# Kernel optimization log

Measured on AMD Instinct MI355X. Metric: run time of the kernel, lower is better.

The kernel has to match this reference:

```python
import jax, jax.numpy as jnp
from jax import lax
import numpy as np

B, W, V, E, H = 512, 40, 12000, 512, 512


def setup_inputs() -> dict:
    key = jax.random.key(0)
    ks = jax.random.split(key, 9)
    s = 0.05
    ques_vec = jax.random.randint(ks[0], (B, W), 0, V + 1)          # token ids, 0 = pad
    ques_len = jax.random.randint(ks[1], (B,), 1, W + 1)             # valid lengths in [1, W]
    lookup_W = jax.random.normal(ks[2], (E, V), jnp.float32) * s     # nn.Linear(vocab, emb).weight
    wih0 = jax.random.normal(ks[3], (2, 4 * H, E), jnp.float32) * s  # [dir, 4H, in]
    whh0 = jax.random.normal(ks[4], (2, 4 * H, H), jnp.float32) * s
    b0 = jax.random.normal(ks[5], (2, 2, 4 * H), jnp.float32) * s    # [dir, {b_ih,b_hh}, 4H]
    wih1 = jax.random.normal(ks[6], (2, 4 * H, 2 * H), jnp.float32) * s
    whh1 = jax.random.normal(ks[7], (2, 4 * H, H), jnp.float32) * s
    b1 = jax.random.normal(ks[8], (2, 2, 4 * H), jnp.float32) * s
    return {"ques_vec": ques_vec, "ques_len": ques_len, "lookup_W": lookup_W,
            "wih0": wih0, "whh0": whh0, "b0": b0,
            "wih1": wih1, "whh1": whh1, "b1": b1}


def _lstm_dir(x, wih, whh, b, reverse):
    # x: [B, T, D]; PyTorch gate order i, f, g, o
    Hc = whh.shape[1]
    xg = jnp.einsum('btd,gd->btg', x, wih) + b[0] + b[1]  # [B, T, 4H]
    xs = jnp.swapaxes(xg, 0, 1)                            # [T, B, 4H]
    if reverse:
        xs = xs[::-1]

    def step(carry, g_t):
        h, c = carry
        g = g_t + h @ whh.T
        i, f, gg, o = jnp.split(g, 4, axis=-1)
        c = jax.nn.sigmoid(f) * c + jax.nn.sigmoid(i) * jnp.tanh(gg)
        h = jax.nn.sigmoid(o) * jnp.tanh(c)
        return (h, c), h

    h0 = jnp.zeros((x.shape[0], Hc), x.dtype)
    _, hs = lax.scan(step, (h0, h0), xs)
    if reverse:
        hs = hs[::-1]
    return jnp.swapaxes(hs, 0, 1)  # [B, T, H]


def _bilstm(x, wih, whh, b):
    fwd = _lstm_dir(x, wih[0], whh[0], b[0], False)
    bwd = _lstm_dir(x, wih[1], whh[1], b[1], True)
    return jnp.concatenate([fwd, bwd], axis=-1)  # [B, T, 2H]


def reference(ques_vec, ques_len, lookup_W, wih0, whh0, b0, wih1, whh1, b1):
    # one-hot over vocab+1 with column 0 dropped == gather with id 0 -> zero vector
    table = jnp.concatenate([jnp.zeros((1, E), lookup_W.dtype), lookup_W.T], axis=0)  # [V+1, E]
    emb = jnp.tanh(table[ques_vec])          # [B, W, E] (dropout=0 -> identity)
    h = _bilstm(emb, wih0, whh0, b0)         # layer 0
    h = _bilstm(h, wih1, whh1, b1)           # layer 1 -> [B, W, 2H]
    # scatter-mask bmm == select hidden state at timestep ques_len-1
    idx = (ques_len - 1)[:, None, None]
    return jnp.take_along_axis(h, idx, axis=1).reshape(ques_vec.shape[0], -1)  # [B, 2H]
```

## Files before the change

### kernel.cpp

```cpp
#include <hip/hip_runtime.h>
#include <hip/hip_bf16.h>
#include <stdint.h>

#define NB 512
#define NW 40
#define NE 512
#define NH 512
#define NV 12000
#define G4 2048

typedef unsigned short u16;
typedef unsigned int u32;
typedef unsigned long long u64;
typedef __attribute__((ext_vector_type(8))) short short8;
typedef __attribute__((ext_vector_type(4))) float f32x4;

__device__ __forceinline__ unsigned short f2bf(float f) {
  unsigned int u = __float_as_uint(f);
  u += 0x7FFF + ((u >> 16) & 1);
  return (unsigned short)(u >> 16);
}
__device__ __forceinline__ float bf2f(unsigned short b) {
  return __uint_as_float(((unsigned int)b) << 16);
}
__device__ __forceinline__ float loadIn(const void* p, long i, int bf) {
  return bf ? bf2f(((const u16*)p)[i]) : ((const float*)p)[i];
}

__global__ void detect_kernel(const u16* p, int* flag) {
  __shared__ int cnt;
  int i = threadIdx.x;
  if (i == 0) cnt = 0;
  __syncthreads();
  unsigned short u = p[2 * (i * 1001)];
  int e = (u >> 7) & 0xFF;
  if (e >= 100 && e <= 126) atomicAdd(&cnt, 1);
  __syncthreads();
  if (i == 0) *flag = (cnt >= 32) ? 1 : 0;
}

__global__ void table_kernel(const void* lookup, const int* flag, u16* tableT) {
  __shared__ float tile[64][65];
  int bf = *flag;
  int v0 = blockIdx.x * 64, e0 = blockIdx.y * 64;
  int tx = threadIdx.x, ty = threadIdx.y;
#pragma unroll
  for (int r = 0; r < 16; ++r) {
    int e = r * 4 + ty, v = tx;
    if (v0 + v < NV)
      tile[e][v] = tanhf(loadIn(lookup, (long)(e0 + e) * NV + v0 + v, bf));
  }
  __syncthreads();
#pragma unroll
  for (int r = 0; r < 16; ++r) {
    int v = r * 4 + ty, e = tx;
    if (v0 + v < NV)
      tableT[(long)(v0 + v) * NE + e0 + e] = f2bf(tile[e][v]);
  }
}

__global__ void embed_kernel(const int* __restrict__ qv,
                             const u16* __restrict__ tableT,
                             u16* __restrict__ emb) {
  int tid = blockIdx.x * 256 + threadIdx.x;
  int token = tid >> 6;
  int chunk = tid & 63;
  int tt = token / NB, b = token % NB;
  int q = qv[b * NW + tt];
  uint4 val = make_uint4(0u, 0u, 0u, 0u);
  if (q > 0) val = *(const uint4*)(tableT + (long)(q - 1) * NE + chunk * 8);
  *(uint4*)(emb + (long)token * NE + chunk * 8) = val;
}

__global__ void pack_kernel(const void* wih0, const void* whh0, const void* b0,
                            const void* wih1, const void* whh1, const void* b1,
                            const int* flag, u16* Wc0, u16* Wc1, float* bsum) {
  const long N0 = 2L * G4 * 1024, N1 = 2L * G4 * 1536;
  long idx = (long)blockIdx.x * 256 + threadIdx.x;
  int bf = *flag;
  if (idx < N0) {
    int d = (int)(idx / (G4 * 1024));
    int rem = (int)(idx % (long)(G4 * 1024));
    int g = rem / 1024, k = rem % 1024;
    float v = (k < 512) ? loadIn(wih0, ((long)d * G4 + g) * 512 + k, bf)
                        : loadIn(whh0, ((long)d * G4 + g) * 512 + (k - 512), bf);
    Wc0[idx] = f2bf(v);
  } else if (idx < N0 + N1) {
    long i2 = idx - N0;
    int d = (int)(i2 / (G4 * 1536));
    int rem = (int)(i2 % (long)(G4 * 1536));
    int g = rem / 1536, k = rem % 1536;
    float v = (k < 1024) ? loadIn(wih1, ((long)d * G4 + g) * 1024 + k, bf)
                         : loadIn(whh1, ((long)d * G4 + g) * 512 + (k - 1024), bf);
    Wc1[i2] = f2bf(v);
  } else if (idx < N0 + N1 + 2L * 2 * G4) {
    long i3 = idx - N0 - N1;
    int layer = (int)(i3 / (2 * G4));
    int d = (int)((i3 / G4) & 1);
    int g = (int)(i3 % G4);
    const void* bb = layer ? b1 : b0;
    float v = loadIn(bb, (long)d * 2 * G4 + g, bf) +
              loadIn(bb, (long)d * 2 * G4 + G4 + g, bf);
    bsum[i3] = v;
  }
}

__global__ void zero_bar(unsigned int* bar) {
  bar[blockIdx.x * 256 + threadIdx.x] = 0u;
}

__global__ __launch_bounds__(256, 2) void xg_gemm(
    const u16* __restrict__ X, int Kx, int Kfull, const u16* __restrict__ Wc,
    const float* __restrict__ bsumL, u16* __restrict__ xg) {
  __shared__ __align__(16) char lds[32768];
  const int tid = threadIdx.x;
  const int lane = tid & 63, wv = tid >> 6;
  const int wm = wv & 1, wn = wv >> 1;
  const int col = lane & 15, quad = lane >> 4;
  const int s = blockIdx.x >> 5, w = blockIdx.x & 31;
  const int bx = (s % 40) * 4 + (w & 3);
  const int by = (s / 40) * 8 + (w >> 2);
  const int tb0 = bx * 128;
  const int d = by >> 4, colb = by & 15, j0 = colb * 32;

  f32x4 zero = {0.f, 0.f, 0.f, 0.f};
  f32x4 acc[4][4];
#pragma unroll
  for (int i = 0; i < 4; ++i)
#pragma unroll
    for (int j = 0; j < 4; ++j) acc[i][j] = zero;

  const int iters = Kx >> 6;
  for (int it = 0; it < iters; ++it) {
    int k0 = it << 6;
#pragma unroll
    for (int p = 0; p < 8; ++p) {
      int c = p * 256 + tid;
      const u16* gsrc;
      if (c < 1024) {
        int r = c >> 3, sl = c & 7;
        int kk = k0 + ((sl * 8) ^ ((r & 7) << 3));
        gsrc = X + (long)(tb0 + r) * Kx + kk;
      } else {
        int cb = c - 1024;
        int r = cb >> 3, sl = cb & 7;
        int kk = k0 + ((sl * 8) ^ ((r & 7) << 3));
        int grow = (r >> 5) * 512 + j0 + (r & 31);
        gsrc = Wc + ((long)d * G4 + grow) * Kfull + kk;
      }
      __builtin_amdgcn_global_load_lds(
          (const __attribute__((address_space(1))) void*)(const void*)gsrc,
          (__attribute__((address_space(3))) void*)(lds + p * 4096 + wv * 1024),
          16, 0, 0);
    }
    __syncthreads();
    const u16* As = (const u16*)lds;
    const u16* Bs = (const u16*)(lds + 16384);
#pragma unroll
    for (int ks = 0; ks < 2; ++ks) {
      short8 afr[4], bfr[4];
#pragma unroll
      for (int mf = 0; mf < 4; ++mf) {
        int rm = wm * 64 + mf * 16 + col;
        int sl = (ks * 32 + quad * 8) ^ ((rm & 7) << 3);
        afr[mf] = *(const short8*)(As + rm * 64 + sl);
      }
#pragma unroll
      for (int nf = 0; nf < 4; ++nf) {
        int br = wn * 64 + nf * 16 + col;
        int sl = (ks * 32 + quad * 8) ^ ((br & 7) << 3);
        bfr[nf] = *(const short8*)(Bs + br * 64 + sl);
      }
#pragma unroll
      for (int mf = 0; mf < 4; ++mf)
#pragma unroll
        for (int nf = 0; nf < 4; ++nf)
          acc[mf][nf] = __builtin_amdgcn_mfma_f32_16x16x32_bf16(
              afr[mf], bfr[nf], acc[mf][nf], 0, 0, 0);
    }
    __syncthreads();
  }

  float bias[4];
#pragma unroll
  for (int nf = 0; nf < 4; ++nf) {
    int n = wn * 64 + nf * 16 + col;
    bias[nf] = bsumL[d * G4 + (n >> 5) * 512 + j0 + (n & 31)];
  }
#pragma unroll
  for (int mf = 0; mf < 4; ++mf)
#pragma unroll
    for (int nf = 0; nf < 4; ++nf) {
      int n = wn * 64 + nf * 16 + col;
      int g = n >> 5, jn = n & 31;
#pragma unroll
      for (int r = 0; r < 4; ++r) {
        int m = wm * 64 + mf * 16 + quad * 4 + r;
        int tb = tb0 + m, t = tb >> 9, b = tb & 511;
        long oi = ((((long)t * 2 + d) * 16 + colb) * 512 + b) * 128 + jn * 4 + g;
        xg[oi] = f2bf(acc[mf][nf][r] + bias[nf]);
      }
    }
}

__global__ __launch_bounds__(256, 1) void lstm_pers(
    const u16* __restrict__ xg, const u16* __restrict__ Wc, int Kfull, int Kx,
    u16* __restrict__ hbuf, u16* __restrict__ h0cat, void* __restrict__ outp,
    const int* __restrict__ qlen, const int* __restrict__ flag,
    unsigned int* bar, int layer) {
  __shared__ __align__(16) char lds[163840];
  const int tid = threadIdx.x;
  const int lane = tid & 63, wv = tid >> 6;
  const int wm = wv & 1, wn = wv >> 1;
  const int col = lane & 15, quad = lane >> 4;
  const int l = blockIdx.x;
  const int colid = l & 31, mi = l >> 5;
  const int colb = colid & 15, j0 = colb * 32, d = colid >> 4;
  const int m0 = mi * 64;
  const int gid = l >> 4;

#pragma unroll
  for (int p = 0; p < 32; ++p) {
    int c = p * 256 + tid;
    int row = c >> 6, rem = c & 63;
    int kc = rem >> 3, sl = rem & 7;
    int grow = (row >> 5) * 512 + j0 + (row & 31);
    int gk = Kx + kc * 64 + ((sl * 8) ^ ((row & 7) << 3));
    const u16* gsrc = Wc + ((long)d * G4 + grow) * Kfull + gk;
    __builtin_amdgcn_global_load_lds(
        (const __attribute__((address_space(1))) void*)(const void*)gsrc,
        (__attribute__((address_space(3))) void*)(lds + p * 4096 + wv * 1024),
        16, 0, 0);
  }
  const u16* Bs = (const u16*)lds;
  char* hstg = lds + 131072;
  u16* hLDS = (u16*)hstg;

  float creg[2][4];
#pragma unroll
  for (int i = 0; i < 2; ++i)
#pragma unroll
    for (int r = 0; r < 4; ++r) creg[i][r] = 0.f;
  const int isbf = *flag;
  f32x4 zero = {0.f, 0.f, 0.f, 0.f};

  __syncthreads();

#pragma unroll 1
  for (int t = 0; t < NW; ++t) {
    const int tq = d ? (NW - 1 - t) : t;

    ushort4 xgv[2][4];
    const u16* xgt = xg + ((((long)tq * 2 + d) * 16 + colb) * 512 + m0) * 128;
#pragma unroll
    for (int mf = 0; mf < 2; ++mf)
#pragma unroll
      for (int r = 0; r < 4; ++r) {
        int m = wm * 32 + mf * 16 + quad * 4 + r;
        xgv[mf][r] = *(const ushort4*)(xgt + m * 128 + (wn * 16 + col) * 4);
      }

    f32x4 acc[2][4];
#pragma unroll
    for (int i = 0; i < 2; ++i)
#pragma unroll
      for (int j = 0; j < 4; ++j) acc[i][j] = zero;

    if (t > 0) {
      const u16* hp =
          hbuf + ((t - 1) & 1) * (2L * NB * NH) + ((long)d * NB + m0) * NH;
      auto stage = [&](int it, int pb) {
        char* dst = hstg + pb * 16384;
#pragma unroll
        for (int p = 0; p < 4; ++p) {
          int c = p * 256 + tid;
          int row = c >> 4, slot = c & 15;
          int half = slot >> 3, ck = slot & 7;
          int kk = it * 128 + half * 64 + ((ck * 8) ^ ((row & 7) << 3));
          const u16* gsrc = hp + (long)row * NH + kk;
          __builtin_amdgcn_global_load_lds(
              (const __attribute__((address_space(1))) void*)(const void*)gsrc,
              (__attribute__((address_space(3))) void*)(dst + p * 4096 +
                                                        wv * 1024),
              16, 0, 16 );
        }
      };
      stage(0, 0);
      __syncthreads();
#pragma unroll 1
      for (int it = 0; it < 4; ++it) {
        if (it + 1 < 4) stage(it + 1, (it + 1) & 1);
        const u16* As = (const u16*)(hstg + (it & 1) * 16384);
#pragma unroll
        for (int ks = 0; ks < 4; ++ks) {
          short8 afr[2], bfr[4];
          const int ksub = ks * 32 + quad * 8;
#pragma unroll
          for (int mf = 0; mf < 2; ++mf) {
            int rm = wm * 32 + mf * 16 + col;
            int sl = (ksub & 63) ^ ((rm & 7) << 3);
            afr[mf] = *(const short8*)(As + rm * 128 + (ksub & 64) + sl);
          }
          const int kc = it * 128 + ksub;
#pragma unroll
          for (int g = 0; g < 4; ++g) {
            int br = g * 32 + wn * 16 + col;
            int sl = (kc & 63) ^ ((br & 7) << 3);
            bfr[g] = *(const short8*)(Bs + br * 512 + (kc & ~63) + sl);
          }
#pragma unroll
          for (int mf = 0; mf < 2; ++mf)
#pragma unroll
            for (int g = 0; g < 4; ++g)
              acc[mf][g] = __builtin_amdgcn_mfma_f32_16x16x32_bf16(
                  afr[mf], bfr[g], acc[mf][g], 0, 0, 0);
        }
        if (it + 1 < 4) __syncthreads();
      }
    }

#pragma unroll
    for (int mf = 0; mf < 2; ++mf)
#pragma unroll
      for (int r = 0; r < 4; ++r) {
        int m = wm * 32 + mf * 16 + quad * 4 + r;
        const u16* xv = (const u16*)&xgv[mf][r];
        float gi = acc[mf][0][r] + bf2f(xv[0]);
        float gf = acc[mf][1][r] + bf2f(xv[1]);
        float gg = acc[mf][2][r] + bf2f(xv[2]);
        float go = acc[mf][3][r] + bf2f(xv[3]);
        float si = 1.f / (1.f + __expf(-gi));
        float sf = 1.f / (1.f + __expf(-gf));
        float so = 1.f / (1.f + __expf(-go));
        float cn = sf * creg[mf][r] + si * tanhf(gg);
        float h = so * tanhf(cn);
        creg[mf][r] = cn;
        hLDS[m * 32 + wn * 16 + col] = f2bf(h);
        if (layer == 1 && !isbf) {
          int bg = m0 + m;
          if (qlen[bg] - 1 == tq)
            ((float*)outp)[(long)bg * (2 * NH) + d * NH + j0 + wn * 16 + col] =
                h;
        }
      }
    __syncthreads();

    u16* hnxt = hbuf + (t & 1) * (2L * NB * NH);
#pragma unroll
    for (int p = 0; p < 4; ++p) {
      int c = p * 256 + tid;
      int m = c >> 4, pr = c & 15;
      u32 hw = ((const u32*)hLDS)[m * 16 + pr];
      int bg = m0 + m, jg = j0 + pr * 2;
      __hip_atomic_store((u32*)(hnxt + ((long)d * NB + bg) * NH + jg), hw,
                         __ATOMIC_RELAXED, __HIP_MEMORY_SCOPE_AGENT);
      if (layer == 0) {
        *(u32*)(h0cat + ((long)tq * NB + bg) * (2 * NH) + d * NH + jg) = hw;
      } else if (isbf && qlen[bg] - 1 == tq) {
        *(u32*)((u16*)outp + (long)bg * (2 * NH) + d * NH + jg) = hw;
      }
    }

    if (t < NW - 1) {
      __syncthreads();
      if (tid == 0) {
        u32* cnt = &bar[gid * 64];
        u32* flg = &bar[1024 + gid * 64];
        unsigned old = __hip_atomic_fetch_add(cnt, 1u, __ATOMIC_RELAXED,
                                              __HIP_MEMORY_SCOPE_AGENT);
        if (old == 16u * (t + 1) - 1u)
          __hip_atomic_store(flg, (unsigned)(t + 1), __ATOMIC_RELAXED,
                             __HIP_MEMORY_SCOPE_AGENT);
        else
          while (__hip_atomic_load(flg, __ATOMIC_RELAXED,
                                   __HIP_MEMORY_SCOPE_AGENT) <
                 (unsigned)(t + 1))
            __builtin_amdgcn_s_sleep(1);
      }
      __syncthreads();
    }
  }
}

extern "C" void kernel_launch(void* const* d_in, const int* in_sizes, int n_in,
                              void* d_out, int out_size, void* d_ws,
                              size_t ws_size, hipStream_t stream) {
  const int* qv = (const int*)d_in[0];
  const int* ql = (const int*)d_in[1];
  const void* lookup = d_in[2];
  const void* wih0 = d_in[3];
  const void* whh0 = d_in[4];
  const void* b0 = d_in[5];
  const void* wih1 = d_in[6];
  const void* whh1 = d_in[7];
  const void* b1 = d_in[8];

  char* ws = (char*)d_ws;
  size_t off = 0;
  int* flag = (int*)ws;                 off += 256;
  unsigned int* bar = (unsigned int*)(ws + off); off += 8192;
  float* bsum = (float*)(ws + off);     off += 2L * 2 * G4 * 4;
  u16* Wc0 = (u16*)(ws + off);          off += 2L * G4 * 1024 * 2;
  u16* Wc1 = (u16*)(ws + off);          off += 2L * G4 * 1536 * 2;
  u16* hbuf = (u16*)(ws + off);         off += 2L * 2 * NB * NH * 2;
  u16* h0cat = (u16*)(ws + off);        off += (size_t)NW * NB * 2 * NH * 2;
  u16* emb = (u16*)(ws + off);          off += (size_t)NW * NB * NE * 2;
  u16* xg = (u16*)(ws + off);           off += (size_t)NW * 2 * 16 * 512 * 128 * 2;
  u16* tableT = h0cat;

  detect_kernel<<<1, 64, 0, stream>>>((const u16*)lookup, flag);
  table_kernel<<<dim3(188, 8), dim3(64, 4), 0, stream>>>(lookup, flag, tableT);
  {
    long total = 2L * G4 * 1024 + 2L * G4 * 1536 + 2L * 2 * G4;
    int blocks = (int)((total + 255) / 256);
    pack_kernel<<<blocks, 256, 0, stream>>>(wih0, whh0, b0, wih1, whh1, b1,
                                            flag, Wc0, Wc1, bsum);
  }
  embed_kernel<<<NW * NB / 4, 256, 0, stream>>>(qv, tableT, emb);

  xg_gemm<<<5120, 256, 0, stream>>>(emb, 512, 1024, Wc0, bsum, xg);
  zero_bar<<<8, 256, 0, stream>>>(bar);
  lstm_pers<<<256, 256, 0, stream>>>(xg, Wc0, 1024, 512, hbuf, h0cat, d_out,
                                     ql, flag, bar, 0);
  xg_gemm<<<5120, 256, 0, stream>>>(h0cat, 1024, 1536, Wc1, bsum + 2 * G4, xg);
  zero_bar<<<8, 256, 0, stream>>>(bar);
  lstm_pers<<<256, 256, 0, stream>>>(xg, Wc1, 1536, 1024, hbuf, h0cat, d_out,
                                     ql, flag, bar, 1);
}
```

Before: 1.000 ms.

## Interleave both LSTM directions per block with per-block flag barrier and register-loaded h

Each block now owns 16 hidden columns for both directions and alternates forward and backward steps. The second direction's work can then overlap the first direction's wait on its barrier. The centralized atomic-counter barrier is replaced by per-block flags that one wave polls with a ballot. Hidden state is loaded straight from global memory into registers instead of being staged through double-buffered LDS. Sigmoid and tanh now use fast reciprocal/exp approximations, trading some accuracy for fewer instructions. The barrier flag layout and the block-to-column mapping change, which relies on the launch and workspace setup matching.

```diff
diff --git a/kernel.cpp b/kernel.cpp
--- a/kernel.cpp
+++ b/kernel.cpp
@@ -25,6 +25,14 @@
 }
 __device__ __forceinline__ float loadIn(const void* p, long i, int bf) {
   return bf ? bf2f(((const u16*)p)[i]) : ((const float*)p)[i];
+}
+__device__ __forceinline__ float fast_tanh(float x) {
+  float ax = __builtin_fabsf(x);
+  float t = 1.f - 2.f * __builtin_amdgcn_rcpf(__expf(ax + ax) + 1.f);
+  return __builtin_copysignf(t, x);
+}
+__device__ __forceinline__ float sigm(float x) {
+  return __builtin_amdgcn_rcpf(1.f + __expf(-x));
 }
 
 __global__ void detect_kernel(const u16* p, int* flag) {
@@ -208,33 +216,32 @@
     u16* __restrict__ hbuf, u16* __restrict__ h0cat, void* __restrict__ outp,
     const int* __restrict__ qlen, const int* __restrict__ flag,
     unsigned int* bar, int layer) {
-  __shared__ __align__(16) char lds[163840];
+  __shared__ __align__(16) char lds[133120];
   const int tid = threadIdx.x;
   const int lane = tid & 63, wv = tid >> 6;
-  const int wm = wv & 1, wn = wv >> 1;
   const int col = lane & 15, quad = lane >> 4;
   const int l = blockIdx.x;
-  const int colid = l & 31, mi = l >> 5;
-  const int colb = colid & 15, j0 = colb * 32, d = colid >> 4;
+  const int colb = l & 31;
+  const int mi = l >> 5;
+  const int j0 = colb * 16;
   const int m0 = mi * 64;
-  const int gid = l >> 4;
 
 #pragma unroll
   for (int p = 0; p < 32; ++p) {
     int c = p * 256 + tid;
     int row = c >> 6, rem = c & 63;
     int kc = rem >> 3, sl = rem & 7;
-    int grow = (row >> 5) * 512 + j0 + (row & 31);
+    int dr = row >> 6;
+    int grow = ((row >> 4) & 3) * 512 + j0 + (row & 15);
     int gk = Kx + kc * 64 + ((sl * 8) ^ ((row & 7) << 3));
-    const u16* gsrc = Wc + ((long)d * G4 + grow) * Kfull + gk;
+    const u16* gsrc = Wc + ((long)dr * G4 + grow) * Kfull + gk;
     __builtin_amdgcn_global_load_lds(
         (const __attribute__((address_space(1))) void*)(const void*)gsrc,
         (__attribute__((address_space(3))) void*)(lds + p * 4096 + wv * 1024),
         16, 0, 0);
   }
   const u16* Bs = (const u16*)lds;
-  char* hstg = lds + 131072;
-  u16* hLDS = (u16*)hstg;
+  u16* hLDS = (u16*)(lds + 131072);
 
   float creg[2][4];
 #pragma unroll
@@ -248,136 +255,112 @@
 
 #pragma unroll 1
   for (int t = 0; t < NW; ++t) {
-    const int tq = d ? (NW - 1 - t) : t;
-
-    ushort4 xgv[2][4];
-    const u16* xgt = xg + ((((long)tq * 2 + d) * 16 + colb) * 512 + m0) * 128;
-#pragma unroll
-    for (int mf = 0; mf < 2; ++mf)
+#pragma unroll
+    for (int d = 0; d < 2; ++d) {
+      const int tq = d ? (NW - 1 - t) : t;
+      const int gid = mi * 2 + d;
+
+      ushort4 xgv[4];
+      const u16* xgt =
+          xg + ((((long)tq * 2 + d) * 16 + (colb >> 1)) * 512 + m0) * 128;
 #pragma unroll
       for (int r = 0; r < 4; ++r) {
-        int m = wm * 32 + mf * 16 + quad * 4 + r;
-        xgv[mf][r] = *(const ushort4*)(xgt + m * 128 + (wn * 16 + col) * 4);
-      }
-
-    f32x4 acc[2][4];
-#pragma unroll
-    for (int i = 0; i < 2; ++i)
-#pragma unroll
-      for (int j = 0; j < 4; ++j) acc[i][j] = zero;
-
-    if (t > 0) {
-      const u16* hp =
-          hbuf + ((t - 1) & 1) * (2L * NB * NH) + ((long)d * NB + m0) * NH;
-      auto stage = [&](int it, int pb) {
-        char* dst = hstg + pb * 16384;
-#pragma unroll
-        for (int p = 0; p < 4; ++p) {
-          int c = p * 256 + tid;
-          int row = c >> 4, slot = c & 15;
-          int half = slot >> 3, ck = slot & 7;
-          int kk = it * 128 + half * 64 + ((ck * 8) ^ ((row & 7) << 3));
-          const u16* gsrc = hp + (long)row * NH + kk;
-          __builtin_amdgcn_global_load_lds(
-              (const __attribute__((address_space(1))) void*)(const void*)gsrc,
-              (__attribute__((address_space(3))) void*)(dst + p * 4096 +
-                                                        wv * 1024),
-              16, 0, 16 );
+        int m = wv * 16 + quad * 4 + r;
+        xgv[r] = *(const ushort4*)(xgt + m * 128 + ((colb & 1) * 16 + col) * 4);
+      }
+
+      f32x4 acc[4];
+#pragma unroll
+      for (int g = 0; g < 4; ++g) acc[g] = zero;
+
+      if (t > 0) {
+        if (wv == 0) {
+          u32* sp = bar + gid * 32 + (lane & 31);
+          while (__ballot((int)(__hip_atomic_load(sp, __ATOMIC_RELAXED,
+                                                  __HIP_MEMORY_SCOPE_AGENT) <
+                                (u32)t)))
+            __builtin_amdgcn_s_sleep(1);
         }
-      };
-      stage(0, 0);
-      __syncthreads();
-#pragma unroll 1
-      for (int it = 0; it < 4; ++it) {
-        if (it + 1 < 4) stage(it + 1, (it + 1) & 1);
-        const u16* As = (const u16*)(hstg + (it & 1) * 16384);
-#pragma unroll
-        for (int ks = 0; ks < 4; ++ks) {
-          short8 afr[2], bfr[4];
-          const int ksub = ks * 32 + quad * 8;
-#pragma unroll
-          for (int mf = 0; mf < 2; ++mf) {
-            int rm = wm * 32 + mf * 16 + col;
-            int sl = (ksub & 63) ^ ((rm & 7) << 3);
-            afr[mf] = *(const short8*)(As + rm * 128 + (ksub & 64) + sl);
+        __syncthreads();
+
+        const u16* hp = hbuf + ((t - 1) & 1) * (2L * NB * NH) +
+                        ((long)d * NB + m0 + wv * 16 + col) * NH;
+        short8 afr[16];
+#pragma unroll
+        for (int it = 0; it < 4; ++it)
+#pragma unroll
+          for (int ks = 0; ks < 4; ++ks) {
+            const u64* p = (const u64*)(hp + it * 128 + ks * 32 + quad * 8);
+            union {
+              short8 v;
+              u64 q[2];
+            } u;
+            u.q[0] = __hip_atomic_load((u64*)p, __ATOMIC_RELAXED,
+                                       __HIP_MEMORY_SCOPE_AGENT);
+            u.q[1] = __hip_atomic_load((u64*)p + 1, __ATOMIC_RELAXED,
+                                       __HIP_MEMORY_SCOPE_AGENT);
+            afr[it * 4 + ks] = u.v;
           }
-          const int kc = it * 128 + ksub;
-#pragma unroll
-          for (int g = 0; g < 4; ++g) {
-            int br = g * 32 + wn * 16 + col;
-            int sl = (kc & 63) ^ ((br & 7) << 3);
-            bfr[g] = *(const short8*)(Bs + br * 512 + (kc & ~63) + sl);
+#pragma unroll
+        for (int it = 0; it < 4; ++it)
+#pragma unroll
+          for (int ks = 0; ks < 4; ++ks) {
+            const int kc = it * 128 + ks * 32 + quad * 8;
+#pragma unroll
+            for (int g = 0; g < 4; ++g) {
+              int br = d * 64 + g * 16 + col;
+              int slb = (kc & 63) ^ ((br & 7) << 3);
+              short8 bfr = *(const short8*)(Bs + br * 512 + (kc & ~63) + slb);
+              acc[g] = __builtin_amdgcn_mfma_f32_16x16x32_bf16(
+                  afr[it * 4 + ks], bfr, acc[g], 0, 0, 0);
+            }
           }
-#pragma unroll
-          for (int mf = 0; mf < 2; ++mf)
-#pragma unroll
-            for (int g = 0; g < 4; ++g)
-              acc[mf][g] = __builtin_amdgcn_mfma_f32_16x16x32_bf16(
-                  afr[mf], bfr[g], acc[mf][g], 0, 0, 0);
-        }
-        if (it + 1 < 4) __syncthreads();
-      }
-    }
-
-#pragma unroll
-    for (int mf = 0; mf < 2; ++mf)
+      }
+
 #pragma unroll
       for (int r = 0; r < 4; ++r) {
-        int m = wm * 32 + mf * 16 + quad * 4 + r;
-        const u16* xv = (const u16*)&xgv[mf][r];
-        float gi = acc[mf][0][r] + bf2f(xv[0]);
-        float gf = acc[mf][1][r] + bf2f(xv[1]);
-        float gg = acc[mf][2][r] + bf2f(xv[2]);
-        float go = acc[mf][3][r] + bf2f(xv[3]);
-        float si = 1.f / (1.f + __expf(-gi));
-        float sf = 1.f / (1.f + __expf(-gf));
-        float so = 1.f / (1.f + __expf(-go));
-        float cn = sf * creg[mf][r] + si * tanhf(gg);
-        float h = so * tanhf(cn);
-        creg[mf][r] = cn;
-        hLDS[m * 32 + wn * 16 + col] = f2bf(h);
+        int m = wv * 16 + quad * 4 + r;
+        float gi = acc[0][r] + bf2f(xgv[r].x);
+        float gf = acc[1][r] + bf2f(xgv[r].y);
+        float gg = acc[2][r] + bf2f(xgv[r].z);
+        float go = acc[3][r] + bf2f(xgv[r].w);
+        float si = sigm(gi);
+        float sf = sigm(gf);
+        float so = sigm(go);
+        float cn = sf * creg[d][r] + si * fast_tanh(gg);
+        float h = so * fast_tanh(cn);
+        creg[d][r] = cn;
+        hLDS[m * 16 + col] = f2bf(h);
         if (layer == 1 && !isbf) {
           int bg = m0 + m;
           if (qlen[bg] - 1 == tq)
-            ((float*)outp)[(long)bg * (2 * NH) + d * NH + j0 + wn * 16 + col] =
-                h;
+            ((float*)outp)[(long)bg * (2 * NH) + d * NH + j0 + col] = h;
         }
       }
-    __syncthreads();
-
-    u16* hnxt = hbuf + (t & 1) * (2L * NB * NH);
-#pragma unroll
-    for (int p = 0; p < 4; ++p) {
-      int c = p * 256 + tid;
-      int m = c >> 4, pr = c & 15;
-      u32 hw = ((const u32*)hLDS)[m * 16 + pr];
-      int bg = m0 + m, jg = j0 + pr * 2;
-      __hip_atomic_store((u32*)(hnxt + ((long)d * NB + bg) * NH + jg), hw,
-                         __ATOMIC_RELAXED, __HIP_MEMORY_SCOPE_AGENT);
-      if (layer == 0) {
-        *(u32*)(h0cat + ((long)tq * NB + bg) * (2 * NH) + d * NH + jg) = hw;
-      } else if (isbf && qlen[bg] - 1 == tq) {
-        *(u32*)((u16*)outp + (long)bg * (2 * NH) + d * NH + jg) = hw;
-      }
-    }
-
-    if (t < NW - 1) {
       __syncthreads();
-      if (tid == 0) {
-        u32* cnt = &bar[gid * 64];
-        u32* flg = &bar[1024 + gid * 64];
-        unsigned old = __hip_atomic_fetch_add(cnt, 1u, __ATOMIC_RELAXED,
-                                              __HIP_MEMORY_SCOPE_AGENT);
-        if (old == 16u * (t + 1) - 1u)
-          __hip_atomic_store(flg, (unsigned)(t + 1), __ATOMIC_RELAXED,
-                             __HIP_MEMORY_SCOPE_AGENT);
-        else
-          while (__hip_atomic_load(flg, __ATOMIC_RELAXED,
-                                   __HIP_MEMORY_SCOPE_AGENT) <
-                 (unsigned)(t + 1))
-            __builtin_amdgcn_s_sleep(1);
-      }
-      __syncthreads();
+
+      u16* hnxt = hbuf + (t & 1) * (2L * NB * NH);
+#pragma unroll
+      for (int p = 0; p < 2; ++p) {
+        int c = p * 256 + tid;
+        int m = c >> 3, pr = c & 7;
+        u32 hw = ((const u32*)hLDS)[m * 8 + pr];
+        int bg = m0 + m, jg = j0 + pr * 2;
+        __hip_atomic_store((u32*)(hnxt + ((long)d * NB + bg) * NH + jg), hw,
+                           __ATOMIC_RELAXED, __HIP_MEMORY_SCOPE_AGENT);
+        if (layer == 0) {
+          *(u32*)(h0cat + ((long)tq * NB + bg) * (2 * NH) + d * NH + jg) = hw;
+        } else if (isbf && qlen[bg] - 1 == tq) {
+          *(u32*)((u16*)outp + (long)bg * (2 * NH) + d * NH + jg) = hw;
+        }
+      }
+
+      if (t < NW - 1) {
+        __syncthreads();
+        if (tid == 0)
+          __hip_atomic_store(bar + gid * 32 + colb, (u32)(t + 1),
+                             __ATOMIC_RELAXED, __HIP_MEMORY_SCOPE_AGENT);
+      }
     }
   }
 }
```

Result: slower. 1.265 ms (+26.5%).

## Fuse input projection GEMM into persistent LSTM kernel with MFMA-fragment layouts

Applied to the files above, without the earlier changes.

Removes the separate xg_gemm kernels and computes each timestep's input-gate projection inside the persistent LSTM kernel, overlapped after the h write and before the grid barrier. Embeddings and layer-0 outputs are written directly in MFMA fragment order, and part of W_ih (or a pre-packed layer-1 slice) is kept in LDS. This trades the xg round trip through HBM for extra per-step MFMA work on the recurrent critical path. It also retiles the blocks to 16 hidden columns by 128 rows with 32 blocks per barrier group, and swaps in rcp-based fast sigmoid and tanh.

```diff
diff --git a/kernel.cpp b/kernel.cpp
--- a/kernel.cpp
+++ b/kernel.cpp
@@ -25,6 +25,14 @@
 }
 __device__ __forceinline__ float loadIn(const void* p, long i, int bf) {
   return bf ? bf2f(((const u16*)p)[i]) : ((const float*)p)[i];
+}
+__device__ __forceinline__ float fast_tanh(float x) {
+  float ax = __builtin_fabsf(x);
+  float t = 1.f - 2.f * __builtin_amdgcn_rcpf(__expf(ax + ax) + 1.f);
+  return __builtin_copysignf(t, x);
+}
+__device__ __forceinline__ float sigm(float x) {
+  return __builtin_amdgcn_rcpf(1.f + __expf(-x));
 }
 
 __global__ void detect_kernel(const u16* p, int* flag) {
@@ -61,21 +69,28 @@
 
 __global__ void embed_kernel(const int* __restrict__ qv,
                              const u16* __restrict__ tableT,
-                             u16* __restrict__ emb) {
-  int tid = blockIdx.x * 256 + threadIdx.x;
-  int token = tid >> 6;
-  int chunk = tid & 63;
-  int tt = token / NB, b = token % NB;
-  int q = qv[b * NW + tt];
+                             u16* __restrict__ embf) {
+  long g = (long)blockIdx.x * 256 + threadIdx.x;
+  int l = (int)(g & 63);
+  int kp = (int)((g >> 6) & 15);
+  int bt = (int)((g >> 10) & 31);
+  int tq = (int)(g >> 15);
+  int col = l & 15, quad = l >> 4;
+  int b = bt * 16 + col;
+  int q = qv[b * NW + tq];
   uint4 val = make_uint4(0u, 0u, 0u, 0u);
-  if (q > 0) val = *(const uint4*)(tableT + (long)(q - 1) * NE + chunk * 8);
-  *(uint4*)(emb + (long)token * NE + chunk * 8) = val;
+  if (q > 0)
+    val = *(const uint4*)(tableT + (long)(q - 1) * NE + kp * 32 + quad * 8);
+  *(uint4*)(embf + g * 8) = val;
 }
 
 __global__ void pack_kernel(const void* wih0, const void* whh0, const void* b0,
                             const void* wih1, const void* whh1, const void* b1,
-                            const int* flag, u16* Wc0, u16* Wc1, float* bsum) {
+                            const int* flag, u16* Wc0, u16* Wc1, float* bsum,
+                            u16* Wx1h) {
   const long N0 = 2L * G4 * 1024, N1 = 2L * G4 * 1536;
+  const long NB2 = 2L * 2 * G4;
+  const long N2 = 2L * 32 * 4 * 16 * 512;
   long idx = (long)blockIdx.x * 256 + threadIdx.x;
   int bf = *flag;
   if (idx < N0) {
@@ -93,7 +108,7 @@
     float v = (k < 1024) ? loadIn(wih1, ((long)d * G4 + g) * 1024 + k, bf)
                          : loadIn(whh1, ((long)d * G4 + g) * 512 + (k - 1024), bf);
     Wc1[i2] = f2bf(v);
-  } else if (idx < N0 + N1 + 2L * 2 * G4) {
+  } else if (idx < N0 + N1 + NB2) {
     long i3 = idx - N0 - N1;
     int layer = (int)(i3 / (2 * G4));
     int d = (int)((i3 / G4) & 1);
@@ -102,6 +117,20 @@
     float v = loadIn(bb, (long)d * 2 * G4 + g, bf) +
               loadIn(bb, (long)d * 2 * G4 + G4 + g, bf);
     bsum[i3] = v;
+  } else if (idx < N0 + N1 + NB2 + N2) {
+    long i4 = idx - N0 - N1 - NB2;
+    int e = (int)(i4 & 7);
+    int l = (int)((i4 >> 3) & 63);
+    int kp = (int)((i4 >> 9) & 15);
+    int g = (int)((i4 >> 13) & 3);
+    int jb = (int)((i4 >> 15) & 31);
+    int d = (int)(i4 >> 20);
+    int col = l & 15, quad = l >> 4;
+    float v = loadIn(wih1,
+                     ((long)d * G4 + g * 512 + jb * 16 + col) * 1024 + 512 +
+                         kp * 32 + quad * 8 + e,
+                     bf);
+    Wx1h[i4] = f2bf(v);
   }
 }
 
@@ -109,132 +138,51 @@
   bar[blockIdx.x * 256 + threadIdx.x] = 0u;
 }
 
-__global__ __launch_bounds__(256, 2) void xg_gemm(
-    const u16* __restrict__ X, int Kx, int Kfull, const u16* __restrict__ Wc,
-    const float* __restrict__ bsumL, u16* __restrict__ xg) {
-  __shared__ __align__(16) char lds[32768];
-  const int tid = threadIdx.x;
-  const int lane = tid & 63, wv = tid >> 6;
-  const int wm = wv & 1, wn = wv >> 1;
-  const int col = lane & 15, quad = lane >> 4;
-  const int s = blockIdx.x >> 5, w = blockIdx.x & 31;
-  const int bx = (s % 40) * 4 + (w & 3);
-  const int by = (s / 40) * 8 + (w >> 2);
-  const int tb0 = bx * 128;
-  const int d = by >> 4, colb = by & 15, j0 = colb * 32;
-
-  f32x4 zero = {0.f, 0.f, 0.f, 0.f};
-  f32x4 acc[4][4];
-#pragma unroll
-  for (int i = 0; i < 4; ++i)
-#pragma unroll
-    for (int j = 0; j < 4; ++j) acc[i][j] = zero;
-
-  const int iters = Kx >> 6;
-  for (int it = 0; it < iters; ++it) {
-    int k0 = it << 6;
-#pragma unroll
-    for (int p = 0; p < 8; ++p) {
-      int c = p * 256 + tid;
-      const u16* gsrc;
-      if (c < 1024) {
-        int r = c >> 3, sl = c & 7;
-        int kk = k0 + ((sl * 8) ^ ((r & 7) << 3));
-        gsrc = X + (long)(tb0 + r) * Kx + kk;
-      } else {
-        int cb = c - 1024;
-        int r = cb >> 3, sl = cb & 7;
-        int kk = k0 + ((sl * 8) ^ ((r & 7) << 3));
-        int grow = (r >> 5) * 512 + j0 + (r & 31);
-        gsrc = Wc + ((long)d * G4 + grow) * Kfull + kk;
-      }
-      __builtin_amdgcn_global_load_lds(
-          (const __attribute__((address_space(1))) void*)(const void*)gsrc,
-          (__attribute__((address_space(3))) void*)(lds + p * 4096 + wv * 1024),
-          16, 0, 0);
-    }
-    __syncthreads();
-    const u16* As = (const u16*)lds;
-    const u16* Bs = (const u16*)(lds + 16384);
-#pragma unroll
-    for (int ks = 0; ks < 2; ++ks) {
-      short8 afr[4], bfr[4];
-#pragma unroll
-      for (int mf = 0; mf < 4; ++mf) {
-        int rm = wm * 64 + mf * 16 + col;
-        int sl = (ks * 32 + quad * 8) ^ ((rm & 7) << 3);
-        afr[mf] = *(const short8*)(As + rm * 64 + sl);
-      }
-#pragma unroll
-      for (int nf = 0; nf < 4; ++nf) {
-        int br = wn * 64 + nf * 16 + col;
-        int sl = (ks * 32 + quad * 8) ^ ((br & 7) << 3);
-        bfr[nf] = *(const short8*)(Bs + br * 64 + sl);
-      }
-#pragma unroll
-      for (int mf = 0; mf < 4; ++mf)
-#pragma unroll
-        for (int nf = 0; nf < 4; ++nf)
-          acc[mf][nf] = __builtin_amdgcn_mfma_f32_16x16x32_bf16(
-              afr[mf], bfr[nf], acc[mf][nf], 0, 0, 0);
-    }
-    __syncthreads();
-  }
-
-  float bias[4];
-#pragma unroll
-  for (int nf = 0; nf < 4; ++nf) {
-    int n = wn * 64 + nf * 16 + col;
-    bias[nf] = bsumL[d * G4 + (n >> 5) * 512 + j0 + (n & 31)];
-  }
-#pragma unroll
-  for (int mf = 0; mf < 4; ++mf)
-#pragma unroll
-    for (int nf = 0; nf < 4; ++nf) {
-      int n = wn * 64 + nf * 16 + col;
-      int g = n >> 5, jn = n & 31;
-#pragma unroll
-      for (int r = 0; r < 4; ++r) {
-        int m = wm * 64 + mf * 16 + quad * 4 + r;
-        int tb = tb0 + m, t = tb >> 9, b = tb & 511;
-        long oi = ((((long)t * 2 + d) * 16 + colb) * 512 + b) * 128 + jn * 4 + g;
-        xg[oi] = f2bf(acc[mf][nf][r] + bias[nf]);
-      }
-    }
-}
-
 __global__ __launch_bounds__(256, 1) void lstm_pers(
-    const u16* __restrict__ xg, const u16* __restrict__ Wc, int Kfull, int Kx,
-    u16* __restrict__ hbuf, u16* __restrict__ h0cat, void* __restrict__ outp,
+    const u16* __restrict__ Xf, int KPX, const u16* __restrict__ Wxh,
+    const u16* __restrict__ Wc, int Kfull, int Kx, u16* __restrict__ hbuf,
+    u16* __restrict__ h0f, void* __restrict__ outp,
     const int* __restrict__ qlen, const int* __restrict__ flag,
-    unsigned int* bar, int layer) {
+    const float* __restrict__ bsumL, unsigned int* bar, int layer) {
   __shared__ __align__(16) char lds[163840];
   const int tid = threadIdx.x;
   const int lane = tid & 63, wv = tid >> 6;
-  const int wm = wv & 1, wn = wv >> 1;
   const int col = lane & 15, quad = lane >> 4;
   const int l = blockIdx.x;
-  const int colid = l & 31, mi = l >> 5;
-  const int colb = colid & 15, j0 = colb * 32, d = colid >> 4;
-  const int m0 = mi * 64;
-  const int gid = l >> 4;
-
-#pragma unroll
-  for (int p = 0; p < 32; ++p) {
-    int c = p * 256 + tid;
-    int row = c >> 6, rem = c & 63;
-    int kc = rem >> 3, sl = rem & 7;
-    int grow = (row >> 5) * 512 + j0 + (row & 31);
-    int gk = Kx + kc * 64 + ((sl * 8) ^ ((row & 7) << 3));
-    const u16* gsrc = Wc + ((long)d * G4 + grow) * Kfull + gk;
-    __builtin_amdgcn_global_load_lds(
-        (const __attribute__((address_space(1))) void*)(const void*)gsrc,
-        (__attribute__((address_space(3))) void*)(lds + p * 4096 + wv * 1024),
-        16, 0, 0);
-  }
-  const u16* Bs = (const u16*)lds;
+  const int cb = l & 31;
+  const int gid = l >> 5;
+  const int d = gid & 1, mi = gid >> 1;
+  const int j0 = cb * 16;
+  const int m0 = mi * 128;
+
+#pragma unroll
+  for (int rg = 0; rg < 2; ++rg) {
+    int base_k = rg ? Kx : 0;
+    char* dstb = lds + rg * 65536;
+#pragma unroll
+    for (int p = 0; p < 16; ++p) {
+      int c = p * 256 + tid;
+      int row = c >> 6, rem = c & 63;
+      int kc = rem >> 3, sl = rem & 7;
+      int gk = base_k + kc * 64 + ((sl * 8) ^ ((row & 7) << 3));
+      const u16* gsrc =
+          Wc + ((long)d * G4 + (row >> 4) * 512 + j0 + (row & 15)) * Kfull + gk;
+      __builtin_amdgcn_global_load_lds(
+          (const __attribute__((address_space(1))) void*)(const void*)gsrc,
+          (__attribute__((address_space(3))) void*)(dstb + p * 4096 +
+                                                    wv * 1024),
+          16, 0, 0);
+    }
+  }
+  const u16* WihS = (const u16*)lds;
+  const u16* WhhS = (const u16*)(lds + 65536);
   char* hstg = lds + 131072;
   u16* hLDS = (u16*)hstg;
+
+  float biasv[4];
+#pragma unroll
+  for (int g = 0; g < 4; ++g)
+    biasv[g] = bsumL[d * G4 + g * 512 + j0 + col];
 
   float creg[2][4];
 #pragma unroll
@@ -243,28 +191,64 @@
     for (int r = 0; r < 4; ++r) creg[i][r] = 0.f;
   const int isbf = *flag;
   f32x4 zero = {0.f, 0.f, 0.f, 0.f};
+  f32x4 accX[2][4];
 
   __syncthreads();
+
+  auto xpart = [&](int tq) {
+#pragma unroll
+    for (int i = 0; i < 2; ++i)
+#pragma unroll
+      for (int g = 0; g < 4; ++g) accX[i][g] = zero;
+    const u16* Ab = Xf + (((long)tq * 32 + mi * 8 + wv * 2) * KPX) * 512 +
+                    lane * 8;
+#pragma unroll 2
+    for (int kp = 0; kp < 16; ++kp) {
+      short8 ax0 = *(const short8*)(Ab + (long)kp * 512);
+      short8 ax1 = *(const short8*)(Ab + ((long)KPX + kp) * 512);
+      int off = (kp & 1) * 32 + quad * 8;
+#pragma unroll
+      for (int g = 0; g < 4; ++g) {
+        int br = g * 16 + col;
+        short8 bx = *(const short8*)(WihS + br * 512 + (kp >> 1) * 64 +
+                                     (off ^ ((br & 7) << 3)));
+        accX[0][g] =
+            __builtin_amdgcn_mfma_f32_16x16x32_bf16(ax0, bx, accX[0][g], 0, 0, 0);
+        accX[1][g] =
+            __builtin_amdgcn_mfma_f32_16x16x32_bf16(ax1, bx, accX[1][g], 0, 0, 0);
+      }
+    }
+    if (KPX > 16) {
+      const u16* WxB =
+          Wxh + (((long)d * 32 + cb) * 4) * 16 * 512 + lane * 8;
+#pragma unroll 2
+      for (int kp = 16; kp < 32; ++kp) {
+        short8 ax0 = *(const short8*)(Ab + (long)kp * 512);
+        short8 ax1 = *(const short8*)(Ab + ((long)KPX + kp) * 512);
+#pragma unroll
+        for (int g = 0; g < 4; ++g) {
+          short8 bx =
+              *(const short8*)(WxB + ((long)g * 16 + (kp - 16)) * 512);
+          accX[0][g] = __builtin_amdgcn_mfma_f32_16x16x32_bf16(ax0, bx,
+                                                               accX[0][g], 0, 0, 0);
+          accX[1][g] = __builtin_amdgcn_mfma_f32_16x16x32_bf16(ax1, bx,
+                                                               accX[1][g], 0, 0, 0);
+        }
+      }
+    }
+  };
+
+  xpart(d ? NW - 1 : 0);
 
 #pragma unroll 1
   for (int t = 0; t < NW; ++t) {
     const int tq = d ? (NW - 1 - t) : t;
 
-    ushort4 xgv[2][4];
-    const u16* xgt = xg + ((((long)tq * 2 + d) * 16 + colb) * 512 + m0) * 128;
-#pragma unroll
-    for (int mf = 0; mf < 2; ++mf)
-#pragma unroll
-      for (int r = 0; r < 4; ++r) {
-        int m = wm * 32 + mf * 16 + quad * 4 + r;
-        xgv[mf][r] = *(const ushort4*)(xgt + m * 128 + (wn * 16 + col) * 4);
-      }
-
-    f32x4 acc[2][4];
+    f32x4 accA[2][4];
 #pragma unroll
     for (int i = 0; i < 2; ++i)
 #pragma unroll
-      for (int j = 0; j < 4; ++j) acc[i][j] = zero;
+      for (int g = 0; g < 4; ++g) accA[i][g] = accX[i][g];
 
     if (t > 0) {
       const u16* hp =
@@ -274,9 +258,8 @@
 #pragma unroll
         for (int p = 0; p < 4; ++p) {
           int c = p * 256 + tid;
-          int row = c >> 4, slot = c & 15;
-          int half = slot >> 3, ck = slot & 7;
-          int kk = it * 128 + half * 64 + ((ck * 8) ^ ((row & 7) << 3));
+          int row = c >> 3, slot = c & 7;
+          int kk = it * 64 + ((slot * 8) ^ ((row & 7) << 3));
           const u16* gsrc = hp + (long)row * NH + kk;
           __builtin_amdgcn_global_load_lds(
               (const __attribute__((address_space(1))) void*)(const void*)gsrc,
@@ -288,34 +271,31 @@
       stage(0, 0);
       __syncthreads();
 #pragma unroll 1
-      for (int it = 0; it < 4; ++it) {
-        if (it + 1 < 4) stage(it + 1, (it + 1) & 1);
+      for (int it = 0; it < 8; ++it) {
+        if (it + 1 < 8) stage(it + 1, (it + 1) & 1);
         const u16* As = (const u16*)(hstg + (it & 1) * 16384);
 #pragma unroll
-        for (int ks = 0; ks < 4; ++ks) {
-          short8 afr[2], bfr[4];
-          const int ksub = ks * 32 + quad * 8;
+        for (int ks = 0; ks < 2; ++ks) {
+          int ksub = ks * 32 + quad * 8;
+          short8 afr[2];
 #pragma unroll
           for (int mf = 0; mf < 2; ++mf) {
-            int rm = wm * 32 + mf * 16 + col;
-            int sl = (ksub & 63) ^ ((rm & 7) << 3);
-            afr[mf] = *(const short8*)(As + rm * 128 + (ksub & 64) + sl);
+            int rm = wv * 32 + mf * 16 + col;
+            afr[mf] = *(const short8*)(As + rm * 64 + (ksub ^ ((rm & 7) << 3)));
           }
-          const int kc = it * 128 + ksub;
+          int kc = it * 64 + ksub;
 #pragma unroll
           for (int g = 0; g < 4; ++g) {
-            int br = g * 32 + wn * 16 + col;
-            int sl = (kc & 63) ^ ((br & 7) << 3);
-            bfr[g] = *(const short8*)(Bs + br * 512 + (kc & ~63) + sl);
+            int br = g * 16 + col;
+            short8 bfr = *(const short8*)(WhhS + br * 512 + (kc & ~63) +
+                                          ((kc & 63) ^ ((br & 7) << 3)));
+            accA[0][g] = __builtin_amdgcn_mfma_f32_16x16x32_bf16(
+                afr[0], bfr, accA[0][g], 0, 0, 0);
+            accA[1][g] = __builtin_amdgcn_mfma_f32_16x16x32_bf16(
+                afr[1], bfr, accA[1][g], 0, 0, 0);
           }
-#pragma unroll
-          for (int mf = 0; mf < 2; ++mf)
-#pragma unroll
-            for (int g = 0; g < 4; ++g)
-              acc[mf][g] = __builtin_amdgcn_mfma_f32_16x16x32_bf16(
-                  afr[mf], bfr[g], acc[mf][g], 0, 0, 0);
         }
-        if (it + 1 < 4) __syncthreads();
+        if (it + 1 < 8) __syncthreads();
       }
     }
 
@@ -323,24 +303,22 @@
     for (int mf = 0; mf < 2; ++mf)
 #pragma unroll
       for (int r = 0; r < 4; ++r) {
-        int m = wm * 32 + mf * 16 + quad * 4 + r;
-        const u16* xv = (const u16*)&xgv[mf][r];
-        float gi = acc[mf][0][r] + bf2f(xv[0]);
-        float gf = acc[mf][1][r] + bf2f(xv[1]);
-        float gg = acc[mf][2][r] + bf2f(xv[2]);
-        float go = acc[mf][3][r] + bf2f(xv[3]);
-        float si = 1.f / (1.f + __expf(-gi));
-        float sf = 1.f / (1.f + __expf(-gf));
-        float so = 1.f / (1.f + __expf(-go));
-        float cn = sf * creg[mf][r] + si * tanhf(gg);
-        float h = so * tanhf(cn);
+        int m = wv * 32 + mf * 16 + quad * 4 + r;
+        float gi = accA[mf][0][r] + biasv[0];
+        float gf = accA[mf][1][r] + biasv[1];
+        float gg = accA[mf][2][r] + biasv[2];
+        float go = accA[mf][3][r] + biasv[3];
+        float si = sigm(gi);
+        float sf = sigm(gf);
+        float so = sigm(go);
+        float cn = sf * creg[mf][r] + si * fast_tanh(gg);
+        float h = so * fast_tanh(cn);
         creg[mf][r] = cn;
-        hLDS[m * 32 + wn * 16 + col] = f2bf(h);
+        hLDS[m * 16 + col] = f2bf(h);
         if (layer == 1 && !isbf) {
           int bg = m0 + m;
           if (qlen[bg] - 1 == tq)
-            ((float*)outp)[(long)bg * (2 * NH) + d * NH + j0 + wn * 16 + col] =
-                h;
+            ((float*)outp)[(long)bg * (2 * NH) + d * NH + j0 + col] = h;
         }
       }
     __syncthreads();
@@ -349,17 +327,26 @@
 #pragma unroll
     for (int p = 0; p < 4; ++p) {
       int c = p * 256 + tid;
-      int m = c >> 4, pr = c & 15;
-      u32 hw = ((const u32*)hLDS)[m * 16 + pr];
-      int bg = m0 + m, jg = j0 + pr * 2;
-      __hip_atomic_store((u32*)(hnxt + ((long)d * NB + bg) * NH + jg), hw,
-                         __ATOMIC_RELAXED, __HIP_MEMORY_SCOPE_AGENT);
-      if (layer == 0) {
-        *(u32*)(h0cat + ((long)tq * NB + bg) * (2 * NH) + d * NH + jg) = hw;
-      } else if (isbf && qlen[bg] - 1 == tq) {
-        *(u32*)((u16*)outp + (long)bg * (2 * NH) + d * NH + jg) = hw;
-      }
-    }
+      int m = c >> 3, pr = c & 7;
+      u32 hw = ((const u32*)hLDS)[m * 8 + pr];
+      int bg = m0 + m;
+      __hip_atomic_store((u32*)(hnxt + ((long)d * NB + bg) * NH + j0 + pr * 2),
+                         hw, __ATOMIC_RELAXED, __HIP_MEMORY_SCOPE_AGENT);
+      if (layer == 1 && isbf && qlen[bg] - 1 == tq)
+        *(u32*)((u16*)outp + (long)bg * (2 * NH) + d * NH + j0 + pr * 2) = hw;
+    }
+    if (layer == 0) {
+      int oct = tid >> 7, m = tid & 127;
+      int k0 = d * 512 + j0 + oct * 8;
+      int kp = k0 >> 5, qd = (k0 >> 3) & 3;
+      int bt = mi * 8 + (m >> 4);
+      const u32* sp = (const u32*)hLDS + m * 8 + oct * 4;
+      uint4 v = make_uint4(sp[0], sp[1], sp[2], sp[3]);
+      *(uint4*)(h0f + (((long)tq * 32 + bt) * 32 + kp) * 512 +
+                (qd * 16 + (m & 15)) * 8) = v;
+    }
+
+    if (t + 1 < NW) xpart(d ? (NW - 2 - t) : (t + 1));
 
     if (t < NW - 1) {
       __syncthreads();
@@ -368,7 +355,7 @@
         u32* flg = &bar[1024 + gid * 64];
         unsigned old = __hip_atomic_fetch_add(cnt, 1u, __ATOMIC_RELAXED,
                                               __HIP_MEMORY_SCOPE_AGENT);
-        if (old == 16u * (t + 1) - 1u)
+        if (old == 32u * (t + 1) - 1u)
           __hip_atomic_store(flg, (unsigned)(t + 1), __ATOMIC_RELAXED,
                              __HIP_MEMORY_SCOPE_AGENT);
         else
@@ -402,28 +389,27 @@
   float* bsum = (float*)(ws + off);     off += 2L * 2 * G4 * 4;
   u16* Wc0 = (u16*)(ws + off);          off += 2L * G4 * 1024 * 2;
   u16* Wc1 = (u16*)(ws + off);          off += 2L * G4 * 1536 * 2;
+  u16* Wx1h = (u16*)(ws + off);         off += 2L * 32 * 4 * 16 * 512 * 2;
   u16* hbuf = (u16*)(ws + off);         off += 2L * 2 * NB * NH * 2;
-  u16* h0cat = (u16*)(ws + off);        off += (size_t)NW * NB * 2 * NH * 2;
-  u16* emb = (u16*)(ws + off);          off += (size_t)NW * NB * NE * 2;
-  u16* xg = (u16*)(ws + off);           off += (size_t)NW * 2 * 16 * 512 * 128 * 2;
-  u16* tableT = h0cat;
+  u16* h0f = (u16*)(ws + off);          off += (size_t)NW * NB * 2 * NH * 2;
+  u16* embf = (u16*)(ws + off);         off += (size_t)NW * NB * NE * 2;
+  u16* tableT = h0f;
 
   detect_kernel<<<1, 64, 0, stream>>>((const u16*)lookup, flag);
   table_kernel<<<dim3(188, 8), dim3(64, 4), 0, stream>>>(lookup, flag, tableT);
   {
-    long total = 2L * G4 * 1024 + 2L * G4 * 1536 + 2L * 2 * G4;
+    long total = 2L * G4 * 1024 + 2L * G4 * 1536 + 2L * 2 * G4 +
+                 2L * 32 * 4 * 16 * 512;
     int blocks = (int)((total + 255) / 256);
     pack_kernel<<<blocks, 256, 0, stream>>>(wih0, whh0, b0, wih1, whh1, b1,
-                                            flag, Wc0, Wc1, bsum);
-  }
-  embed_kernel<<<NW * NB / 4, 256, 0, stream>>>(qv, tableT, emb);
-
-  xg_gemm<<<5120, 256, 0, stream>>>(emb, 512, 1024, Wc0, bsum, xg);
+                                            flag, Wc0, Wc1, bsum, Wx1h);
+  }
+  embed_kernel<<<5120, 256, 0, stream>>>(qv, tableT, embf);
+
   zero_bar<<<8, 256, 0, stream>>>(bar);
-  lstm_pers<<<256, 256, 0, stream>>>(xg, Wc0, 1024, 512, hbuf, h0cat, d_out,
-                                     ql, flag, bar, 0);
-  xg_gemm<<<5120, 256, 0, stream>>>(h0cat, 1024, 1536, Wc1, bsum + 2 * G4, xg);
+  lstm_pers<<<256, 256, 0, stream>>>(embf, 16, Wx1h, Wc0, 1024, 512, hbuf, h0f,
+                                     d_out, ql, flag, bsum, bar, 0);
   zero_bar<<<8, 256, 0, stream>>>(bar);
-  lstm_pers<<<256, 256, 0, stream>>>(xg, Wc1, 1536, 1024, hbuf, h0cat, d_out,
-                                     ql, flag, bar, 1);
-}
+  lstm_pers<<<256, 256, 0, stream>>>(h0f, 32, Wx1h, Wc1, 1536, 1024, hbuf, h0f,
+                                     d_out, ql, flag, bsum + 2 * G4, bar, 1);
+}
```

After: 1.195 ms. 19.5% more time.

## Restage recurrent h tile in halves, use fast gate math, defer side stores past barrier

Applied to the files above, without the earlier changes.

The recurrent h@Whh step now stages the h tile in two 256-wide halves instead of four double-buffered 128-wide chunks. This halves the number of stage/sync rounds, and MFMAs are issued right after each B-fragment load to cut register pressure. Sigmoid and tanh switch to exp plus a hardware reciprocal approximation. Stores of layer-0 outputs and final outputs are moved after the inter-block grid barrier, taking them off the critical path of the sequential recurrence. The trade-offs are lost overlap between staging and compute, and slightly less accurate activations.

```diff
diff --git a/kernel.cpp b/kernel.cpp
--- a/kernel.cpp
+++ b/kernel.cpp
@@ -25,6 +25,14 @@
 }
 __device__ __forceinline__ float loadIn(const void* p, long i, int bf) {
   return bf ? bf2f(((const u16*)p)[i]) : ((const float*)p)[i];
+}
+__device__ __forceinline__ float fast_tanh(float x) {
+  float ax = __builtin_fabsf(x);
+  float t = 1.f - 2.f * __builtin_amdgcn_rcpf(__expf(ax + ax) + 1.f);
+  return __builtin_copysignf(t, x);
+}
+__device__ __forceinline__ float sigm(float x) {
+  return __builtin_amdgcn_rcpf(1.f + __expf(-x));
 }
 
 __global__ void detect_kernel(const u16* p, int* flag) {
@@ -269,53 +277,49 @@
     if (t > 0) {
       const u16* hp =
           hbuf + ((t - 1) & 1) * (2L * NB * NH) + ((long)d * NB + m0) * NH;
-      auto stage = [&](int it, int pb) {
-        char* dst = hstg + pb * 16384;
-#pragma unroll
-        for (int p = 0; p < 4; ++p) {
+      auto stageH = [&](int half) {
+#pragma unroll
+        for (int p = 0; p < 8; ++p) {
           int c = p * 256 + tid;
-          int row = c >> 4, slot = c & 15;
-          int half = slot >> 3, ck = slot & 7;
-          int kk = it * 128 + half * 64 + ((ck * 8) ^ ((row & 7) << 3));
+          int row = c >> 5, slot = c & 31;
+          int kk = half * 256 + (slot >> 3) * 64 +
+                   (((slot & 7) * 8) ^ ((row & 7) << 3));
           const u16* gsrc = hp + (long)row * NH + kk;
           __builtin_amdgcn_global_load_lds(
               (const __attribute__((address_space(1))) void*)(const void*)gsrc,
-              (__attribute__((address_space(3))) void*)(dst + p * 4096 +
+              (__attribute__((address_space(3))) void*)(hstg + p * 4096 +
                                                         wv * 1024),
               16, 0, 16 );
         }
       };
-      stage(0, 0);
-      __syncthreads();
+      const u16* As = (const u16*)hstg;
 #pragma unroll 1
-      for (int it = 0; it < 4; ++it) {
-        if (it + 1 < 4) stage(it + 1, (it + 1) & 1);
-        const u16* As = (const u16*)(hstg + (it & 1) * 16384);
-#pragma unroll
-        for (int ks = 0; ks < 4; ++ks) {
-          short8 afr[2], bfr[4];
+      for (int half = 0; half < 2; ++half) {
+        stageH(half);
+        __syncthreads();
+#pragma unroll
+        for (int ks = 0; ks < 8; ++ks) {
           const int ksub = ks * 32 + quad * 8;
+          short8 afr[2];
 #pragma unroll
           for (int mf = 0; mf < 2; ++mf) {
             int rm = wm * 32 + mf * 16 + col;
-            int sl = (ksub & 63) ^ ((rm & 7) << 3);
-            afr[mf] = *(const short8*)(As + rm * 128 + (ksub & 64) + sl);
+            afr[mf] = *(const short8*)(As + rm * 256 + (ksub & ~63) +
+                                       ((ksub & 63) ^ ((rm & 7) << 3)));
           }
-          const int kc = it * 128 + ksub;
+          const int kc = half * 256 + ksub;
 #pragma unroll
           for (int g = 0; g < 4; ++g) {
             int br = g * 32 + wn * 16 + col;
-            int sl = (kc & 63) ^ ((br & 7) << 3);
-            bfr[g] = *(const short8*)(Bs + br * 512 + (kc & ~63) + sl);
+            int slb = (kc & 63) ^ ((br & 7) << 3);
+            short8 bfr = *(const short8*)(Bs + br * 512 + (kc & ~63) + slb);
+#pragma unroll
+            for (int mf = 0; mf < 2; ++mf)
+              acc[mf][g] = __builtin_amdgcn_mfma_f32_16x16x32_bf16(
+                  afr[mf], bfr, acc[mf][g], 0, 0, 0);
           }
-#pragma unroll
-          for (int mf = 0; mf < 2; ++mf)
-#pragma unroll
-            for (int g = 0; g < 4; ++g)
-              acc[mf][g] = __builtin_amdgcn_mfma_f32_16x16x32_bf16(
-                  afr[mf], bfr[g], acc[mf][g], 0, 0, 0);
         }
-        if (it + 1 < 4) __syncthreads();
+        __syncthreads();
       }
     }
 
@@ -329,11 +333,11 @@
         float gf = acc[mf][1][r] + bf2f(xv[1]);
         float gg = acc[mf][2][r] + bf2f(xv[2]);
         float go = acc[mf][3][r] + bf2f(xv[3]);
-        float si = 1.f / (1.f + __expf(-gi));
-        float sf = 1.f / (1.f + __expf(-gf));
-        float so = 1.f / (1.f + __expf(-go));
-        float cn = sf * creg[mf][r] + si * tanhf(gg);
-        float h = so * tanhf(cn);
+        float si = sigm(gi);
+        float sf = sigm(gf);
+        float so = sigm(go);
+        float cn = sf * creg[mf][r] + si * fast_tanh(gg);
+        float h = so * fast_tanh(cn);
         creg[mf][r] = cn;
         hLDS[m * 32 + wn * 16 + col] = f2bf(h);
         if (layer == 1 && !isbf) {
@@ -346,19 +350,18 @@
     __syncthreads();
 
     u16* hnxt = hbuf + (t & 1) * (2L * NB * NH);
+    u32 hw[4];
+    int bgp[4], jgp[4];
 #pragma unroll
     for (int p = 0; p < 4; ++p) {
       int c = p * 256 + tid;
       int m = c >> 4, pr = c & 15;
-      u32 hw = ((const u32*)hLDS)[m * 16 + pr];
-      int bg = m0 + m, jg = j0 + pr * 2;
-      __hip_atomic_store((u32*)(hnxt + ((long)d * NB + bg) * NH + jg), hw,
-                         __ATOMIC_RELAXED, __HIP_MEMORY_SCOPE_AGENT);
-      if (layer == 0) {
-        *(u32*)(h0cat + ((long)tq * NB + bg) * (2 * NH) + d * NH + jg) = hw;
-      } else if (isbf && qlen[bg] - 1 == tq) {
-        *(u32*)((u16*)outp + (long)bg * (2 * NH) + d * NH + jg) = hw;
-      }
+      hw[p] = ((const u32*)hLDS)[m * 16 + pr];
+      bgp[p] = m0 + m;
+      jgp[p] = j0 + pr * 2;
+      __hip_atomic_store(
+          (u32*)(hnxt + ((long)d * NB + bgp[p]) * NH + jgp[p]), hw[p],
+          __ATOMIC_RELAXED, __HIP_MEMORY_SCOPE_AGENT);
     }
 
     if (t < NW - 1) {
@@ -379,6 +382,17 @@
       }
       __syncthreads();
     }
+
+#pragma unroll
+    for (int p = 0; p < 4; ++p) {
+      if (layer == 0) {
+        *(u32*)(h0cat + ((long)tq * NB + bgp[p]) * (2 * NH) + d * NH +
+                jgp[p]) = hw[p];
+      } else if (isbf && qlen[bgp[p]] - 1 == tq) {
+        *(u32*)((u16*)outp + (long)bgp[p] * (2 * NH) + d * NH + jgp[p]) =
+            hw[p];
+      }
+    }
   }
 }
 
```

Measured after the change: 949.2 us. 1.05x faster.
